# Performance work log

Measured on AMD Instinct MI355X. Metric: run time of the kernel, lower is better.

Reference implementation:

```python
import jax, jax.numpy as jnp
import numpy as np

NUM_HEADS = 16
EPS = 1e-5


def setup_inputs() -> dict:
    key = jax.random.key(0)
    ks = jax.random.split(key, 9)
    B, S, D = 2, 2048, 1024
    s = 1.0 / np.sqrt(D)
    return {
        "x": jax.random.normal(ks[0], (B, S, D), dtype=jnp.float32),
        "Wq": jax.random.uniform(ks[1], (D, D), jnp.float32, -s, s),
        "bq": jax.random.uniform(ks[2], (D,), jnp.float32, -s, s),
        "Wk": jax.random.uniform(ks[3], (D, D), jnp.float32, -s, s),
        "bk": jax.random.uniform(ks[4], (D,), jnp.float32, -s, s),
        "Wv": jax.random.uniform(ks[5], (D, D), jnp.float32, -s, s),
        "bv": jax.random.uniform(ks[6], (D,), jnp.float32, -s, s),
        "Wo": jax.random.uniform(ks[7], (D, D), jnp.float32, -s, s),
        "bo": jax.random.uniform(ks[8], (D,), jnp.float32, -s, s),
    }


def reference(x, Wq, bq, Wk, bk, Wv, bv, Wo, bo):
    B, S, D = x.shape
    H = NUM_HEADS
    hd = D // H
    # projections -> [B, H, S, hd]
    def proj(W, b):
        return (x @ W + b).reshape(B, S, H, hd).transpose(0, 2, 1, 3)
    Q = proj(Wq, bq)
    K = proj(Wk, bk)
    V = proj(Wv, bv)
    scores = jnp.einsum("bhqd,bhkd->bhqk", Q, K) / jnp.sqrt(jnp.float32(hd))
    attn = jax.nn.softmax(scores, axis=-1)  # dropout is identity in eval mode
    out = jnp.einsum("bhqk,bhkd->bhqd", attn, V)
    out = out.transpose(0, 2, 1, 3).reshape(B, S, D)
    out = jax.nn.relu(out @ Wo + bo)
    mu = jnp.mean(out, axis=-1, keepdims=True)
    var = jnp.var(out, axis=-1, keepdims=True)
    return (out - mu) * jax.lax.rsqrt(var + EPS)
```

## Files before the change

kernel.cpp:

```cpp
#include <hip/hip_runtime.h>
#include <hip/hip_bf16.h>
#include <math.h>

#define Bb 2
#define Ss 2048
#define Dd 1024
#define Hh 16
#define HD 64
#define Mm (Bb*Ss)

typedef __attribute__((ext_vector_type(8))) short bf8_t;
typedef __attribute__((ext_vector_type(4))) float f4_t;
typedef __attribute__((ext_vector_type(2))) unsigned u2_t;

#define LOG2E 1.4426950408889634f

#define AS1 __attribute__((address_space(1)))
#define AS3 __attribute__((address_space(3)))

__device__ __forceinline__ void gl2lds16(const void* g, void* l) {
    __builtin_amdgcn_global_load_lds((const AS1 unsigned int*)g,
                                     (AS3 unsigned int*)l, 16, 0, 0);
}
__device__ __forceinline__ short bfr(float f) {
    __hip_bfloat16 h = __float2bfloat16(f);
    return *reinterpret_cast<short*>(&h);
}
__device__ __forceinline__ unsigned pkbf16(float a, float b) {
    const unsigned ua = __builtin_bit_cast(unsigned, a) + 0x8000u;
    const unsigned ub = __builtin_bit_cast(unsigned, b) + 0x8000u;
    return __builtin_amdgcn_perm(ub, ua, 0x07060302u);
}
__device__ __forceinline__ float fexp2(float x) {
    return __builtin_amdgcn_exp2f(x);
}

__global__ __launch_bounds__(256)
void prep(const float* __restrict__ x,
          const float* __restrict__ w0, const float* __restrict__ w1,
          const float* __restrict__ w2, const float* __restrict__ w3,
          __hip_bfloat16* __restrict__ Wt4, __hip_bfloat16* __restrict__ Xh)
{
    const int z = blockIdx.z;
    if (z < 4) {
        const float* W = (z == 0) ? w0 : (z == 1) ? w1 : (z == 2) ? w2 : w3;
        __hip_bfloat16* Wt = Wt4 + (size_t)z * Dd * Dd;
        __shared__ float t[32][33];
        const int n0 = blockIdx.x * 32, k0 = blockIdx.y * 32;
        const int tx = threadIdx.x & 31, ty = threadIdx.x >> 5;
        #pragma unroll
        for (int rr = 0; rr < 4; ++rr)
            t[ty + rr*8][tx] = W[(size_t)(k0 + ty + rr*8) * Dd + n0 + tx];
        __syncthreads();
        #pragma unroll
        for (int rr = 0; rr < 4; ++rr)
            Wt[(size_t)(n0 + ty + rr*8) * Dd + k0 + tx] =
                __float2bfloat16(t[tx][ty + rr*8]);
    } else {
        const int bid = (z - 4) * 1024 + blockIdx.y * 32 + blockIdx.x;
        const size_t i = ((size_t)bid * 256 + threadIdx.x) * 8;
        const float4 a = *(const float4*)&x[i];
        const float4 b = *(const float4*)&x[i + 4];
        bf8_t o;
        o[0] = bfr(a.x); o[1] = bfr(a.y); o[2] = bfr(a.z); o[3] = bfr(a.w);
        o[4] = bfr(b.x); o[5] = bfr(b.y); o[6] = bfr(b.z); o[7] = bfr(b.w);
        *(bf8_t*)&Xh[i] = o;
    }
}

__global__ __launch_bounds__(256)
void gemm_qkv(const __hip_bfloat16* __restrict__ A,
              const __hip_bfloat16* __restrict__ Bt,
              const float* __restrict__ b0, const float* __restrict__ b1,
              const float* __restrict__ b2,
              __hip_bfloat16* __restrict__ Qh, __hip_bfloat16* __restrict__ Kh,
              __hip_bfloat16* __restrict__ Vt)
{
    __shared__ __align__(16) char pool[34816];
    __hip_bfloat16* As = (__hip_bfloat16*)pool;
    __hip_bfloat16* Bs = As + 2 * 128 * 32;

    const int tid  = threadIdx.x;
    const int wave = tid >> 6;
    const int lane = tid & 63;
    const int llo  = lane & 15;
    const int lhi  = lane >> 4;
    const int wm   = wave & 1;
    const int wn   = wave >> 1;
    const int row0 = blockIdx.y * 128;
    const int col0 = blockIdx.x * 128;

    size_t aoff[2], boff[2];
    int    loff[2];
    #pragma unroll
    for (int p = 0; p < 2; ++p) {
        const int g = p * 256 + wave * 64 + lane;
        const int r = g >> 2, kc = (g & 3) * 8;
        aoff[p] = (size_t)(row0 + r) * Dd + kc;
        boff[p] = (size_t)(col0 + r) * Dd + kc;
        loff[p] = (p * 256 + wave * 64) * 16;
    }
    const __hip_bfloat16* Acur = A;
    const __hip_bfloat16* Bcur = Bt;

    auto stage = [&](int buf) {
        #pragma unroll
        for (int p = 0; p < 2; ++p) {
            gl2lds16(Acur + aoff[p], (char*)As + buf*8192 + loff[p]);
            gl2lds16(Bcur + boff[p], (char*)Bs + buf*8192 + loff[p]);
        }
        Acur += 32; Bcur += 32;
    };

    f4_t acc[4][4] = {};
    stage(0);
    for (int kt = 0; kt < 32; ++kt) {
        const int buf = kt & 1;
        __syncthreads();
        if (kt + 1 < 32) stage(buf ^ 1);

        bf8_t a[4], b[4];
        #pragma unroll
        for (int i = 0; i < 4; ++i)
            a[i] = *(const bf8_t*)&As[buf*4096 + (wm*64 + i*16 + llo) * 32 + lhi*8];
        #pragma unroll
        for (int j = 0; j < 4; ++j)
            b[j] = *(const bf8_t*)&Bs[buf*4096 + (wn*64 + j*16 + llo) * 32 + lhi*8];
        #pragma unroll
        for (int i = 0; i < 4; ++i)
            #pragma unroll
            for (int j = 0; j < 4; ++j)
                acc[i][j] = __builtin_amdgcn_mfma_f32_16x16x32_bf16(
                    a[i], b[j], acc[i][j], 0, 0, 0);
    }

    const int sel   = col0 >> 10;
    const int cbase = col0 & 1023;
    if (sel < 2) {
        const float scale = (sel == 0) ? 0.125f * LOG2E : 1.0f;
        const float* bp = (sel == 0) ? b0 : b1;
        __hip_bfloat16* outQK = (sel == 0) ? Qh : Kh;
        #pragma unroll
        for (int i = 0; i < 4; ++i) {
            #pragma unroll
            for (int r = 0; r < 4; ++r) {
                const int m  = row0 + wm*64 + i*16 + lhi*4 + r;
                const int b_ = m >> 11, s_ = m & (Ss - 1);
                #pragma unroll
                for (int j = 0; j < 4; ++j) {
                    const int col = cbase + wn*64 + j*16 + llo;
                    const int h_  = col >> 6, e_ = col & 63;
                    const float v = (acc[i][j][r] + bp[col]) * scale;
                    outQK[((size_t)(b_*Hh + h_)*Ss + s_)*HD + e_] = __float2bfloat16(v);
                }
            }
        }
    } else {
        __syncthreads();
        __hip_bfloat16* Ls = (__hip_bfloat16*)pool;
        float bv[4];
        #pragma unroll
        for (int j = 0; j < 4; ++j) bv[j] = b2[cbase + wn*64 + j*16 + llo];
        #pragma unroll
        for (int i = 0; i < 4; ++i)
            #pragma unroll
            for (int r = 0; r < 4; ++r) {
                const int ml = wm*64 + i*16 + lhi*4 + r;
                #pragma unroll
                for (int j = 0; j < 4; ++j)
                    Ls[(wn*64 + j*16 + llo)*136 + ml] =
                        __float2bfloat16(acc[i][j][r] + bv[j]);
            }
        __syncthreads();
        const int b_ = row0 >> 11;
        const int sb = row0 & (Ss - 1);
        #pragma unroll
        for (int p = 0; p < 8; ++p) {
            const int cl = p*16 + (tid >> 4);
            const int m  = (tid & 15) * 8;
            const bf8_t v = *(const bf8_t*)&Ls[cl*136 + m];
            const int cc = cbase + cl;
            *(bf8_t*)&Vt[((size_t)(b_*Hh + (cc >> 6))*HD + (cc & 63))*Ss + sb + m] = v;
        }
    }
}

__global__ __launch_bounds__(128, 2)
void attn_mfma(const __hip_bfloat16* __restrict__ Qh,
               const __hip_bfloat16* __restrict__ Kh,
               const __hip_bfloat16* __restrict__ Vt,
               __hip_bfloat16* __restrict__ Ah)
{
    const int b    = blockIdx.z;
    const int h    = blockIdx.y;
    const int wave = threadIdx.x >> 6;
    const int lane = threadIdx.x & 63;
    const int llo  = lane & 15;
    const int lhi  = lane >> 4;
    const int qb   = blockIdx.x * 64 + wave * 32;

    const size_t base = ((size_t)(b*Hh + h)) * Ss * HD;

    __shared__ __hip_bfloat16 Ks[2][2 * 64 * 32];
    __shared__ __hip_bfloat16 Vs[2][2 * 64 * 32];
    __shared__ __hip_bfloat16 Pl[2][32 * 64];
    __hip_bfloat16* Pw = &Pl[wave][0];

    int koff[4], voff[4], loff[4];
    #pragma unroll
    for (int it = 0; it < 4; ++it) {
        const int g  = it*128 + wave*64 + lane;
        const int hf = g >> 8;
        const int rr = (g >> 2) & 63;
        const int c8 = (g & 3) * 8;
        koff[it] = rr*HD + hf*32 + c8;
        voff[it] = rr*Ss + hf*32 + c8;
        loff[it] = (it*128 + wave*64) * 16;
    }
    const __hip_bfloat16* Kcur = Kh + base;
    const __hip_bfloat16* Vcur = Vt + base;

    auto stage = [&](int buf) {
        #pragma unroll
        for (int it = 0; it < 4; ++it) {
            gl2lds16(Kcur + koff[it], (char*)&Ks[buf][0] + loff[it]);
            gl2lds16(Vcur + voff[it], (char*)&Vs[buf][0] + loff[it]);
        }
        Kcur += 64 * HD;
        Vcur += 64;
    };

    bf8_t qf[2][2];
    #pragma unroll
    for (int s = 0; s < 2; ++s)
        #pragma unroll
        for (int d = 0; d < 2; ++d)
            qf[s][d] = *(const bf8_t*)&Qh[base + (size_t)(qb + 16*s + llo)*HD + 32*d + lhi*8];

    f4_t o_[2][4];
    float lacc[2];
    #pragma unroll
    for (int s = 0; s < 2; ++s) {
        #pragma unroll
        for (int n = 0; n < 4; ++n) o_[s][n] = (f4_t){0.f,0.f,0.f,0.f};
        lacc[s] = 0.f;
    }

    const f4_t zf = {0.f,0.f,0.f,0.f};
    const int llo7 = llo & 7;

    stage(0);

    for (int t = 0; t < Ss/64; ++t) {
        const int buf = t & 1;
        __syncthreads();
        if (t + 1 < Ss/64) stage(buf ^ 1);

        bf8_t kf[4][2];
        #pragma unroll
        for (int kc = 0; kc < 4; ++kc)
            #pragma unroll
            for (int d = 0; d < 2; ++d)
                kf[kc][d] = *(const bf8_t*)&Ks[buf][d*2048 + (kc*16 + llo)*32 + lhi*8];

        f4_t sacc[2][4];
        #pragma unroll
        for (int s = 0; s < 2; ++s)
            #pragma unroll
            for (int kc = 0; kc < 4; ++kc) {
                sacc[s][kc] = __builtin_amdgcn_mfma_f32_16x16x32_bf16(kf[kc][0], qf[s][0], zf, 0, 0, 0);
                sacc[s][kc] = __builtin_amdgcn_mfma_f32_16x16x32_bf16(kf[kc][1], qf[s][1], sacc[s][kc], 0, 0, 0);
            }

        #pragma unroll
        for (int s = 0; s < 2; ++s) {
            #pragma unroll
            for (int kc = 0; kc < 4; ++kc) {
                const float p0 = fexp2(sacc[s][kc][0]);
                const float p1 = fexp2(sacc[s][kc][1]);
                const float p2 = fexp2(sacc[s][kc][2]);
                const float p3 = fexp2(sacc[s][kc][3]);
                lacc[s] += (p0 + p1) + (p2 + p3);
                const u2_t pk = { pkbf16(p0, p1), pkbf16(p2, p3) };
                const int phys = (2*kc + (lhi >> 1)) ^ llo7;
                *(u2_t*)&Pw[(16*s + llo)*64 + phys*8 + (lhi & 1)*4] = pk;
            }
        }
        asm volatile("s_waitcnt lgkmcnt(0)" ::: "memory");

        #pragma unroll
        for (int d = 0; d < 2; ++d) {
            bf8_t pf[2];
            #pragma unroll
            for (int s = 0; s < 2; ++s)
                pf[s] = *(const bf8_t*)&Pw[(16*s + llo)*64 + (((4*d + lhi) ^ llo7) << 3)];
            #pragma unroll
            for (int nc = 0; nc < 4; ++nc) {
                const bf8_t vf = *(const bf8_t*)&Vs[buf][d*2048 + (nc*16 + llo)*32 + lhi*8];
                #pragma unroll
                for (int s = 0; s < 2; ++s)
                    o_[s][nc] = __builtin_amdgcn_mfma_f32_16x16x32_bf16(pf[s], vf, o_[s][nc], 0, 0, 0);
            }
        }
    }

    #pragma unroll
    for (int s = 0; s < 2; ++s) {
        lacc[s] += __shfl_xor(lacc[s], 16);
        lacc[s] += __shfl_xor(lacc[s], 32);
    }

    #pragma unroll
    for (int s = 0; s < 2; ++s) {
        #pragma unroll
        for (int r = 0; r < 4; ++r) {
            const float lv  = __shfl(lacc[s], 4*lhi + r);
            const float inv = 1.0f / lv;
            const int q = qb + 16*s + 4*lhi + r;
            __hip_bfloat16* orow = &Ah[((size_t)(b*Ss) + q)*Dd + h*HD + llo];
            #pragma unroll
            for (int nc = 0; nc < 4; ++nc)
                orow[16*nc] = __float2bfloat16(o_[s][nc][r] * inv);
        }
    }
}

__global__ __launch_bounds__(256)
void gemm_out(const __hip_bfloat16* __restrict__ A,
              const __hip_bfloat16* __restrict__ Bt,
              const float* __restrict__ bias, float* __restrict__ Ro)
{
    __shared__ __hip_bfloat16 As[2][64 * 32];
    __shared__ __hip_bfloat16 Bs[2][64 * 32];

    const int tid  = threadIdx.x;
    const int wave = tid >> 6;
    const int lane = tid & 63;
    const int llo  = lane & 15;
    const int lhi  = lane >> 4;
    const int wm   = wave & 1;
    const int wn   = wave >> 1;
    const int row0 = blockIdx.y * 64;
    const int col0 = blockIdx.x * 64;

    const int gr = tid >> 2, gkc = (tid & 3) * 8;
    const size_t aoff = (size_t)(row0 + gr) * Dd + gkc;
    const size_t boff = (size_t)(col0 + gr) * Dd + gkc;
    const int loff = (wave * 64) * 16;
    const __hip_bfloat16* Acur = A;
    const __hip_bfloat16* Bcur = Bt;

    auto stage = [&](int buf) {
        gl2lds16(Acur + aoff, (char*)&As[buf][0] + loff);
        gl2lds16(Bcur + boff, (char*)&Bs[buf][0] + loff);
        Acur += 32; Bcur += 32;
    };

    f4_t acc[2][2] = {};
    stage(0);
    for (int kt = 0; kt < 32; ++kt) {
        const int buf = kt & 1;
        __syncthreads();
        if (kt + 1 < 32) stage(buf ^ 1);

        bf8_t a[2], b[2];
        #pragma unroll
        for (int i = 0; i < 2; ++i)
            a[i] = *(const bf8_t*)&As[buf][(wm*32 + i*16 + llo) * 32 + lhi*8];
        #pragma unroll
        for (int j = 0; j < 2; ++j)
            b[j] = *(const bf8_t*)&Bs[buf][(wn*32 + j*16 + llo) * 32 + lhi*8];
        #pragma unroll
        for (int i = 0; i < 2; ++i)
            #pragma unroll
            for (int j = 0; j < 2; ++j)
                acc[i][j] = __builtin_amdgcn_mfma_f32_16x16x32_bf16(
                    a[i], b[j], acc[i][j], 0, 0, 0);
    }

    #pragma unroll
    for (int i = 0; i < 2; ++i) {
        #pragma unroll
        for (int r = 0; r < 4; ++r) {
            const int m = row0 + wm*32 + i*16 + lhi*4 + r;
            #pragma unroll
            for (int j = 0; j < 2; ++j) {
                const int col = col0 + wn*32 + j*16 + llo;
                Ro[(size_t)m * Dd + col] = fmaxf(acc[i][j][r] + bias[col], 0.0f);
            }
        }
    }
}

__global__ __launch_bounds__(256)
void layernorm(const float* __restrict__ X, float* __restrict__ out)
{
    const int row = blockIdx.x;
    const float4 v = ((const float4*)(X + (size_t)row*Dd))[threadIdx.x];
    float s  = v.x + v.y + v.z + v.w;
    float ss = v.x*v.x + v.y*v.y + v.z*v.z + v.w*v.w;
    #pragma unroll
    for (int off = 32; off > 0; off >>= 1) {
        s  += __shfl_down(s,  off);
        ss += __shfl_down(ss, off);
    }
    __shared__ float rs[4], rss[4];
    const int wid = threadIdx.x >> 6, lid = threadIdx.x & 63;
    if (lid == 0) { rs[wid] = s; rss[wid] = ss; }
    __syncthreads();
    s  = rs[0] + rs[1] + rs[2] + rs[3];
    ss = rss[0] + rss[1] + rss[2] + rss[3];
    const float mean = s * (1.0f / Dd);
    const float var  = ss * (1.0f / Dd) - mean * mean;
    const float rstd = rsqrtf(var + 1e-5f);
    float4 o;
    o.x = (v.x - mean) * rstd;
    o.y = (v.y - mean) * rstd;
    o.z = (v.z - mean) * rstd;
    o.w = (v.w - mean) * rstd;
    ((float4*)(out + (size_t)row*Dd))[threadIdx.x] = o;
}

extern "C" void kernel_launch(void* const* d_in, const int* in_sizes, int n_in,
                              void* d_out, int out_size, void* d_ws, size_t ws_size,
                              hipStream_t stream)
{
    const float* x  = (const float*)d_in[0];
    const float* Wq = (const float*)d_in[1];
    const float* bq = (const float*)d_in[2];
    const float* Wk = (const float*)d_in[3];
    const float* bk = (const float*)d_in[4];
    const float* Wv = (const float*)d_in[5];
    const float* bv = (const float*)d_in[6];
    const float* Wo = (const float*)d_in[7];
    const float* bo = (const float*)d_in[8];
    float* out = (float*)d_out;

    __hip_bfloat16* Xh    = (__hip_bfloat16*)d_ws;
    __hip_bfloat16* Wqkvt = Xh    + (size_t)Mm*Dd;
    __hip_bfloat16* Wot   = Wqkvt + (size_t)3*Dd*Dd;
    __hip_bfloat16* Ah    = Wot   + (size_t)Dd*Dd;
    __hip_bfloat16* Qh    = Ah    + (size_t)Mm*Dd;
    __hip_bfloat16* Kh    = Qh    + (size_t)Mm*Dd;
    __hip_bfloat16* Vt    = Kh    + (size_t)Mm*Dd;
    float*          Rb    = (float*)Qh;

    prep<<<dim3(32, 32, 6), dim3(256), 0, stream>>>(x, Wq, Wk, Wv, Wo, Wqkvt, Xh);
    gemm_qkv<<<dim3(3*Dd/128, Mm/128), dim3(256), 0, stream>>>(
        Xh, Wqkvt, bq, bk, bv, Qh, Kh, Vt);
    attn_mfma<<<dim3(Ss/64, Hh, Bb), dim3(128), 0, stream>>>(Qh, Kh, Vt, Ah);
    gemm_out<<<dim3(Dd/64, Mm/64), dim3(256), 0, stream>>>(Ah, Wot, bo, Rb);
    layernorm<<<dim3(Mm), dim3(256), 0, stream>>>(Rb, out);
}
```

Measured before the change: 221.5 us.

## Shrink attention tiles to 16 queries per wave and stage Q/K output via LDS

The attention kernel now gives each wave 16 query rows instead of 32 and steps through keys in 32-wide tiles instead of 64. This halves LDS and register use per block, allowing more resident blocks (launch bound raised to 4) and twice as many blocks in the grid. The cost is less reuse of K/V per load and twice as many loop iterations and barriers. Separately, the QKV GEMM epilogue for Q and K now goes through a shared-memory transpose so global stores are 16-byte vectors rather than scattered 2-byte writes.

```diff
diff --git a/kernel.cpp b/kernel.cpp
--- a/kernel.cpp
+++ b/kernel.cpp
@@ -136,31 +136,40 @@
 
     const int sel   = col0 >> 10;
     const int cbase = col0 & 1023;
+    __hip_bfloat16* Ls = (__hip_bfloat16*)pool;
+    __syncthreads();
+
+    float bv[4];
+    const float* bp = (sel == 0) ? b0 : (sel == 1) ? b1 : b2;
+    #pragma unroll
+    for (int j = 0; j < 4; ++j) bv[j] = bp[cbase + wn*64 + j*16 + llo];
+    const float scale = (sel == 0) ? 0.125f * LOG2E : 1.0f;
+
     if (sel < 2) {
-        const float scale = (sel == 0) ? 0.125f * LOG2E : 1.0f;
-        const float* bp = (sel == 0) ? b0 : b1;
+        #pragma unroll
+        for (int i = 0; i < 4; ++i)
+            #pragma unroll
+            for (int r = 0; r < 4; ++r) {
+                const int ml = wm*64 + i*16 + lhi*4 + r;
+                #pragma unroll
+                for (int j = 0; j < 4; ++j)
+                    Ls[ml*136 + wn*64 + j*16 + llo] =
+                        __float2bfloat16((acc[i][j][r] + bv[j]) * scale);
+            }
+        __syncthreads();
         __hip_bfloat16* outQK = (sel == 0) ? Qh : Kh;
         #pragma unroll
-        for (int i = 0; i < 4; ++i) {
-            #pragma unroll
-            for (int r = 0; r < 4; ++r) {
-                const int m  = row0 + wm*64 + i*16 + lhi*4 + r;
-                const int b_ = m >> 11, s_ = m & (Ss - 1);
-                #pragma unroll
-                for (int j = 0; j < 4; ++j) {
-                    const int col = cbase + wn*64 + j*16 + llo;
-                    const int h_  = col >> 6, e_ = col & 63;
-                    const float v = (acc[i][j][r] + bp[col]) * scale;
-                    outQK[((size_t)(b_*Hh + h_)*Ss + s_)*HD + e_] = __float2bfloat16(v);
-                }
-            }
+        for (int p = 0; p < 8; ++p) {
+            const int id = p*256 + tid;
+            const int rl = id >> 4;
+            const int c8 = (id & 15) * 8;
+            const bf8_t v = *(const bf8_t*)&Ls[rl*136 + c8];
+            const int m  = row0 + rl;
+            const int b_ = m >> 11, s_ = m & (Ss - 1);
+            const int col = cbase + c8;
+            *(bf8_t*)&outQK[((size_t)(b_*Hh + (col >> 6))*Ss + s_)*HD + (col & 63)] = v;
         }
     } else {
-        __syncthreads();
-        __hip_bfloat16* Ls = (__hip_bfloat16*)pool;
-        float bv[4];
-        #pragma unroll
-        for (int j = 0; j < 4; ++j) bv[j] = b2[cbase + wn*64 + j*16 + llo];
         #pragma unroll
         for (int i = 0; i < 4; ++i)
             #pragma unroll
@@ -185,7 +194,7 @@
     }
 }
 
-__global__ __launch_bounds__(128, 2)
+__global__ __launch_bounds__(128, 4)
 void attn_mfma(const __hip_bfloat16* __restrict__ Qh,
                const __hip_bfloat16* __restrict__ Kh,
                const __hip_bfloat16* __restrict__ Vt,
@@ -197,24 +206,21 @@
     const int lane = threadIdx.x & 63;
     const int llo  = lane & 15;
     const int lhi  = lane >> 4;
-    const int qb   = blockIdx.x * 64 + wave * 32;
+    const int qb   = blockIdx.x * 32 + wave * 16;
 
     const size_t base = ((size_t)(b*Hh + h)) * Ss * HD;
 
-    __shared__ __hip_bfloat16 Ks[2][2 * 64 * 32];
-    __shared__ __hip_bfloat16 Vs[2][2 * 64 * 32];
-    __shared__ __hip_bfloat16 Pl[2][32 * 64];
+    __shared__ __hip_bfloat16 Ks[2][2 * 32 * 32];
+    __shared__ __hip_bfloat16 Vs[2][64 * 32];
+    __shared__ __hip_bfloat16 Pl[2][16 * 36];
     __hip_bfloat16* Pw = &Pl[wave][0];
 
-    int koff[4], voff[4], loff[4];
-    #pragma unroll
-    for (int it = 0; it < 4; ++it) {
-        const int g  = it*128 + wave*64 + lane;
-        const int hf = g >> 8;
-        const int rr = (g >> 2) & 63;
-        const int c8 = (g & 3) * 8;
-        koff[it] = rr*HD + hf*32 + c8;
-        voff[it] = rr*Ss + hf*32 + c8;
+    int koff[2], voff[2], loff[2];
+    #pragma unroll
+    for (int it = 0; it < 2; ++it) {
+        const int g = it*128 + wave*64 + lane;
+        koff[it] = ((g >> 2) & 31)*HD + (g >> 7)*32 + (g & 3)*8;
+        voff[it] = (g >> 2)*Ss + (g & 3)*8;
         loff[it] = (it*128 + wave*64) * 16;
     }
     const __hip_bfloat16* Kcur = Kh + base;
@@ -222,106 +228,79 @@
 
     auto stage = [&](int buf) {
         #pragma unroll
-        for (int it = 0; it < 4; ++it) {
+        for (int it = 0; it < 2; ++it) {
             gl2lds16(Kcur + koff[it], (char*)&Ks[buf][0] + loff[it]);
             gl2lds16(Vcur + voff[it], (char*)&Vs[buf][0] + loff[it]);
         }
-        Kcur += 64 * HD;
-        Vcur += 64;
+        Kcur += 32 * HD;
+        Vcur += 32;
     };
 
-    bf8_t qf[2][2];
-    #pragma unroll
-    for (int s = 0; s < 2; ++s)
-        #pragma unroll
-        for (int d = 0; d < 2; ++d)
-            qf[s][d] = *(const bf8_t*)&Qh[base + (size_t)(qb + 16*s + llo)*HD + 32*d + lhi*8];
-
-    f4_t o_[2][4];
-    float lacc[2];
-    #pragma unroll
-    for (int s = 0; s < 2; ++s) {
-        #pragma unroll
-        for (int n = 0; n < 4; ++n) o_[s][n] = (f4_t){0.f,0.f,0.f,0.f};
-        lacc[s] = 0.f;
-    }
+    bf8_t qf[2];
+    #pragma unroll
+    for (int d = 0; d < 2; ++d)
+        qf[d] = *(const bf8_t*)&Qh[base + (size_t)(qb + llo)*HD + 32*d + lhi*8];
+
+    f4_t o_[4];
+    float lacc = 0.f;
+    #pragma unroll
+    for (int n = 0; n < 4; ++n) o_[n] = (f4_t){0.f,0.f,0.f,0.f};
 
     const f4_t zf = {0.f,0.f,0.f,0.f};
-    const int llo7 = llo & 7;
 
     stage(0);
 
-    for (int t = 0; t < Ss/64; ++t) {
+    for (int t = 0; t < Ss/32; ++t) {
         const int buf = t & 1;
         __syncthreads();
-        if (t + 1 < Ss/64) stage(buf ^ 1);
-
-        bf8_t kf[4][2];
-        #pragma unroll
-        for (int kc = 0; kc < 4; ++kc)
+        if (t + 1 < Ss/32) stage(buf ^ 1);
+
+        bf8_t kf[2][2];
+        #pragma unroll
+        for (int kc = 0; kc < 2; ++kc)
             #pragma unroll
             for (int d = 0; d < 2; ++d)
-                kf[kc][d] = *(const bf8_t*)&Ks[buf][d*2048 + (kc*16 + llo)*32 + lhi*8];
-
-        f4_t sacc[2][4];
-        #pragma unroll
-        for (int s = 0; s < 2; ++s)
-            #pragma unroll
-            for (int kc = 0; kc < 4; ++kc) {
-                sacc[s][kc] = __builtin_amdgcn_mfma_f32_16x16x32_bf16(kf[kc][0], qf[s][0], zf, 0, 0, 0);
-                sacc[s][kc] = __builtin_amdgcn_mfma_f32_16x16x32_bf16(kf[kc][1], qf[s][1], sacc[s][kc], 0, 0, 0);
-            }
-
-        #pragma unroll
-        for (int s = 0; s < 2; ++s) {
-            #pragma unroll
-            for (int kc = 0; kc < 4; ++kc) {
-                const float p0 = fexp2(sacc[s][kc][0]);
-                const float p1 = fexp2(sacc[s][kc][1]);
-                const float p2 = fexp2(sacc[s][kc][2]);
-                const float p3 = fexp2(sacc[s][kc][3]);
-                lacc[s] += (p0 + p1) + (p2 + p3);
-                const u2_t pk = { pkbf16(p0, p1), pkbf16(p2, p3) };
-                const int phys = (2*kc + (lhi >> 1)) ^ llo7;
-                *(u2_t*)&Pw[(16*s + llo)*64 + phys*8 + (lhi & 1)*4] = pk;
-            }
+                kf[kc][d] = *(const bf8_t*)&Ks[buf][d*1024 + (kc*16 + llo)*32 + lhi*8];
+
+        f4_t sacc[2];
+        #pragma unroll
+        for (int kc = 0; kc < 2; ++kc) {
+            sacc[kc] = __builtin_amdgcn_mfma_f32_16x16x32_bf16(kf[kc][0], qf[0], zf, 0, 0, 0);
+            sacc[kc] = __builtin_amdgcn_mfma_f32_16x16x32_bf16(kf[kc][1], qf[1], sacc[kc], 0, 0, 0);
+        }
+
+        #pragma unroll
+        for (int kc = 0; kc < 2; ++kc) {
+            const float p0 = fexp2(sacc[kc][0]);
+            const float p1 = fexp2(sacc[kc][1]);
+            const float p2 = fexp2(sacc[kc][2]);
+            const float p3 = fexp2(sacc[kc][3]);
+            lacc += (p0 + p1) + (p2 + p3);
+            const u2_t pk = { pkbf16(p0, p1), pkbf16(p2, p3) };
+            *(u2_t*)&Pw[llo*36 + kc*16 + lhi*4] = pk;
         }
         asm volatile("s_waitcnt lgkmcnt(0)" ::: "memory");
 
-        #pragma unroll
-        for (int d = 0; d < 2; ++d) {
-            bf8_t pf[2];
-            #pragma unroll
-            for (int s = 0; s < 2; ++s)
-                pf[s] = *(const bf8_t*)&Pw[(16*s + llo)*64 + (((4*d + lhi) ^ llo7) << 3)];
-            #pragma unroll
-            for (int nc = 0; nc < 4; ++nc) {
-                const bf8_t vf = *(const bf8_t*)&Vs[buf][d*2048 + (nc*16 + llo)*32 + lhi*8];
-                #pragma unroll
-                for (int s = 0; s < 2; ++s)
-                    o_[s][nc] = __builtin_amdgcn_mfma_f32_16x16x32_bf16(pf[s], vf, o_[s][nc], 0, 0, 0);
-            }
-        }
-    }
-
-    #pragma unroll
-    for (int s = 0; s < 2; ++s) {
-        lacc[s] += __shfl_xor(lacc[s], 16);
-        lacc[s] += __shfl_xor(lacc[s], 32);
-    }
-
-    #pragma unroll
-    for (int s = 0; s < 2; ++s) {
-        #pragma unroll
-        for (int r = 0; r < 4; ++r) {
-            const float lv  = __shfl(lacc[s], 4*lhi + r);
-            const float inv = 1.0f / lv;
-            const int q = qb + 16*s + 4*lhi + r;
-            __hip_bfloat16* orow = &Ah[((size_t)(b*Ss) + q)*Dd + h*HD + llo];
-            #pragma unroll
-            for (int nc = 0; nc < 4; ++nc)
-                orow[16*nc] = __float2bfloat16(o_[s][nc][r] * inv);
-        }
+        const bf8_t pf = *(const bf8_t*)&Pw[llo*36 + lhi*8];
+        #pragma unroll
+        for (int nc = 0; nc < 4; ++nc) {
+            const bf8_t vf = *(const bf8_t*)&Vs[buf][(nc*16 + llo)*32 + lhi*8];
+            o_[nc] = __builtin_amdgcn_mfma_f32_16x16x32_bf16(pf, vf, o_[nc], 0, 0, 0);
+        }
+    }
+
+    lacc += __shfl_xor(lacc, 16);
+    lacc += __shfl_xor(lacc, 32);
+
+    #pragma unroll
+    for (int r = 0; r < 4; ++r) {
+        const float lv  = __shfl(lacc, 4*lhi + r);
+        const float inv = 1.0f / lv;
+        const int q = qb + 4*lhi + r;
+        __hip_bfloat16* orow = &Ah[((size_t)(b*Ss) + q)*Dd + h*HD + llo];
+        #pragma unroll
+        for (int nc = 0; nc < 4; ++nc)
+            orow[16*nc] = __float2bfloat16(o_[nc][r] * inv);
     }
 }
 
@@ -448,7 +427,7 @@
     prep<<<dim3(32, 32, 6), dim3(256), 0, stream>>>(x, Wq, Wk, Wv, Wo, Wqkvt, Xh);
     gemm_qkv<<<dim3(3*Dd/128, Mm/128), dim3(256), 0, stream>>>(
         Xh, Wqkvt, bq, bk, bv, Qh, Kh, Vt);
-    attn_mfma<<<dim3(Ss/64, Hh, Bb), dim3(128), 0, stream>>>(Qh, Kh, Vt, Ah);
+    attn_mfma<<<dim3(Ss/32, Hh, Bb), dim3(128), 0, stream>>>(Qh, Kh, Vt, Ah);
     gemm_out<<<dim3(Dd/64, Mm/64), dim3(256), 0, stream>>>(Ah, Wot, bo, Rb);
     layernorm<<<dim3(Mm), dim3(256), 0, stream>>>(Rb, out);
 }
```

Result: slower. 239.8 us (+8.3%).

## Stage Q/K stores via LDS and split-K retile output GEMM with fused epilogue

Applied to the files above, without the earlier changes.

The Q/K epilogue of the QKV GEMM now goes through an LDS transpose buffer, so each thread writes 16-byte coalesced vectors into the head-major layout instead of scattered scalar stores. The output projection moves from 64x64 to 128x128 tiles with a two-way split-K over blockIdx.z. Each split writes raw fp32 partials, and layernorm sums them and applies bias and ReLU. This improves data reuse and store coalescing, at the cost of extra partial-sum traffic and more workspace.

```diff
diff --git a/kernel.cpp b/kernel.cpp
--- a/kernel.cpp
+++ b/kernel.cpp
@@ -136,31 +136,40 @@
 
     const int sel   = col0 >> 10;
     const int cbase = col0 & 1023;
+    __hip_bfloat16* Ls = (__hip_bfloat16*)pool;
+    __syncthreads();
+
+    float bv[4];
+    const float* bp = (sel == 0) ? b0 : (sel == 1) ? b1 : b2;
+    #pragma unroll
+    for (int j = 0; j < 4; ++j) bv[j] = bp[cbase + wn*64 + j*16 + llo];
+    const float scale = (sel == 0) ? 0.125f * LOG2E : 1.0f;
+
     if (sel < 2) {
-        const float scale = (sel == 0) ? 0.125f * LOG2E : 1.0f;
-        const float* bp = (sel == 0) ? b0 : b1;
+        #pragma unroll
+        for (int i = 0; i < 4; ++i)
+            #pragma unroll
+            for (int r = 0; r < 4; ++r) {
+                const int ml = wm*64 + i*16 + lhi*4 + r;
+                #pragma unroll
+                for (int j = 0; j < 4; ++j)
+                    Ls[ml*136 + wn*64 + j*16 + llo] =
+                        __float2bfloat16((acc[i][j][r] + bv[j]) * scale);
+            }
+        __syncthreads();
         __hip_bfloat16* outQK = (sel == 0) ? Qh : Kh;
         #pragma unroll
-        for (int i = 0; i < 4; ++i) {
-            #pragma unroll
-            for (int r = 0; r < 4; ++r) {
-                const int m  = row0 + wm*64 + i*16 + lhi*4 + r;
-                const int b_ = m >> 11, s_ = m & (Ss - 1);
-                #pragma unroll
-                for (int j = 0; j < 4; ++j) {
-                    const int col = cbase + wn*64 + j*16 + llo;
-                    const int h_  = col >> 6, e_ = col & 63;
-                    const float v = (acc[i][j][r] + bp[col]) * scale;
-                    outQK[((size_t)(b_*Hh + h_)*Ss + s_)*HD + e_] = __float2bfloat16(v);
-                }
-            }
+        for (int p = 0; p < 8; ++p) {
+            const int id = p*256 + tid;
+            const int rl = id >> 4;
+            const int c8 = (id & 15) * 8;
+            const bf8_t v = *(const bf8_t*)&Ls[rl*136 + c8];
+            const int m  = row0 + rl;
+            const int b_ = m >> 11, s_ = m & (Ss - 1);
+            const int col = cbase + c8;
+            *(bf8_t*)&outQK[((size_t)(b_*Hh + (col >> 6))*Ss + s_)*HD + (col & 63)] = v;
         }
     } else {
-        __syncthreads();
-        __hip_bfloat16* Ls = (__hip_bfloat16*)pool;
-        float bv[4];
-        #pragma unroll
-        for (int j = 0; j < 4; ++j) bv[j] = b2[cbase + wn*64 + j*16 + llo];
         #pragma unroll
         for (int i = 0; i < 4; ++i)
             #pragma unroll
@@ -328,10 +337,10 @@
 __global__ __launch_bounds__(256)
 void gemm_out(const __hip_bfloat16* __restrict__ A,
               const __hip_bfloat16* __restrict__ Bt,
-              const float* __restrict__ bias, float* __restrict__ Ro)
-{
-    __shared__ __hip_bfloat16 As[2][64 * 32];
-    __shared__ __hip_bfloat16 Bs[2][64 * 32];
+              float* __restrict__ Ro)
+{
+    __shared__ __hip_bfloat16 As[2][128 * 32];
+    __shared__ __hip_bfloat16 Bs[2][128 * 32];
 
     const int tid  = threadIdx.x;
     const int wave = tid >> 6;
@@ -340,63 +349,84 @@
     const int lhi  = lane >> 4;
     const int wm   = wave & 1;
     const int wn   = wave >> 1;
-    const int row0 = blockIdx.y * 64;
-    const int col0 = blockIdx.x * 64;
-
-    const int gr = tid >> 2, gkc = (tid & 3) * 8;
-    const size_t aoff = (size_t)(row0 + gr) * Dd + gkc;
-    const size_t boff = (size_t)(col0 + gr) * Dd + gkc;
-    const int loff = (wave * 64) * 16;
-    const __hip_bfloat16* Acur = A;
-    const __hip_bfloat16* Bcur = Bt;
+    const int row0 = blockIdx.y * 128;
+    const int col0 = blockIdx.x * 128;
+    const int z    = blockIdx.z;
+
+    size_t aoff[2], boff[2];
+    int    loff[2];
+    #pragma unroll
+    for (int p = 0; p < 2; ++p) {
+        const int g = p * 256 + wave * 64 + lane;
+        const int r = g >> 2, kc = (g & 3) * 8;
+        aoff[p] = (size_t)(row0 + r) * Dd + kc;
+        boff[p] = (size_t)(col0 + r) * Dd + kc;
+        loff[p] = (p * 256 + wave * 64) * 16;
+    }
+    const __hip_bfloat16* Acur = A  + (size_t)z * (Dd/2);
+    const __hip_bfloat16* Bcur = Bt + (size_t)z * (Dd/2);
 
     auto stage = [&](int buf) {
-        gl2lds16(Acur + aoff, (char*)&As[buf][0] + loff);
-        gl2lds16(Bcur + boff, (char*)&Bs[buf][0] + loff);
+        #pragma unroll
+        for (int p = 0; p < 2; ++p) {
+            gl2lds16(Acur + aoff[p], (char*)&As[buf][0] + loff[p]);
+            gl2lds16(Bcur + boff[p], (char*)&Bs[buf][0] + loff[p]);
+        }
         Acur += 32; Bcur += 32;
     };
 
-    f4_t acc[2][2] = {};
+    f4_t acc[4][4] = {};
     stage(0);
-    for (int kt = 0; kt < 32; ++kt) {
+    for (int kt = 0; kt < 16; ++kt) {
         const int buf = kt & 1;
         __syncthreads();
-        if (kt + 1 < 32) stage(buf ^ 1);
-
-        bf8_t a[2], b[2];
-        #pragma unroll
-        for (int i = 0; i < 2; ++i)
-            a[i] = *(const bf8_t*)&As[buf][(wm*32 + i*16 + llo) * 32 + lhi*8];
-        #pragma unroll
-        for (int j = 0; j < 2; ++j)
-            b[j] = *(const bf8_t*)&Bs[buf][(wn*32 + j*16 + llo) * 32 + lhi*8];
-        #pragma unroll
-        for (int i = 0; i < 2; ++i)
-            #pragma unroll
-            for (int j = 0; j < 2; ++j)
+        if (kt + 1 < 16) stage(buf ^ 1);
+
+        bf8_t a[4], b[4];
+        #pragma unroll
+        for (int i = 0; i < 4; ++i)
+            a[i] = *(const bf8_t*)&As[buf][(wm*64 + i*16 + llo) * 32 + lhi*8];
+        #pragma unroll
+        for (int j = 0; j < 4; ++j)
+            b[j] = *(const bf8_t*)&Bs[buf][(wn*64 + j*16 + llo) * 32 + lhi*8];
+        #pragma unroll
+        for (int i = 0; i < 4; ++i)
+            #pragma unroll
+            for (int j = 0; j < 4; ++j)
                 acc[i][j] = __builtin_amdgcn_mfma_f32_16x16x32_bf16(
                     a[i], b[j], acc[i][j], 0, 0, 0);
     }
 
-    #pragma unroll
-    for (int i = 0; i < 2; ++i) {
+    float* Roz = Ro + (size_t)z * Mm * Dd;
+    #pragma unroll
+    for (int i = 0; i < 4; ++i) {
         #pragma unroll
         for (int r = 0; r < 4; ++r) {
-            const int m = row0 + wm*32 + i*16 + lhi*4 + r;
-            #pragma unroll
-            for (int j = 0; j < 2; ++j) {
-                const int col = col0 + wn*32 + j*16 + llo;
-                Ro[(size_t)m * Dd + col] = fmaxf(acc[i][j][r] + bias[col], 0.0f);
+            const int m = row0 + wm*64 + i*16 + lhi*4 + r;
+            #pragma unroll
+            for (int j = 0; j < 4; ++j) {
+                const int col = col0 + wn*64 + j*16 + llo;
+                Roz[(size_t)m * Dd + col] = acc[i][j][r];
             }
         }
     }
 }
 
 __global__ __launch_bounds__(256)
-void layernorm(const float* __restrict__ X, float* __restrict__ out)
+void layernorm(const float* __restrict__ P0, const float* __restrict__ P1,
+               const float* __restrict__ bias, float* __restrict__ out)
 {
     const int row = blockIdx.x;
-    const float4 v = ((const float4*)(X + (size_t)row*Dd))[threadIdx.x];
+    const int c = threadIdx.x;
+    const float4 a  = ((const float4*)(P0 + (size_t)row*Dd))[c];
+    const float4 b  = ((const float4*)(P1 + (size_t)row*Dd))[c];
+    const float4 bb = ((const float4*)bias)[c];
+    float4 v;
+    v.x = fmaxf(a.x + b.x + bb.x, 0.0f);
+    v.y = fmaxf(a.y + b.y + bb.y, 0.0f);
+    v.z = fmaxf(a.z + b.z + bb.z, 0.0f);
+    v.w = fmaxf(a.w + b.w + bb.w, 0.0f);
+
     float s  = v.x + v.y + v.z + v.w;
     float ss = v.x*v.x + v.y*v.y + v.z*v.z + v.w*v.w;
     #pragma unroll
@@ -405,7 +435,7 @@
         ss += __shfl_down(ss, off);
     }
     __shared__ float rs[4], rss[4];
-    const int wid = threadIdx.x >> 6, lid = threadIdx.x & 63;
+    const int wid = c >> 6, lid = c & 63;
     if (lid == 0) { rs[wid] = s; rss[wid] = ss; }
     __syncthreads();
     s  = rs[0] + rs[1] + rs[2] + rs[3];
@@ -418,7 +448,7 @@
     o.y = (v.y - mean) * rstd;
     o.z = (v.z - mean) * rstd;
     o.w = (v.w - mean) * rstd;
-    ((float4*)(out + (size_t)row*Dd))[threadIdx.x] = o;
+    ((float4*)(out + (size_t)row*Dd))[c] = o;
 }
 
 extern "C" void kernel_launch(void* const* d_in, const int* in_sizes, int n_in,
@@ -449,6 +479,6 @@
     gemm_qkv<<<dim3(3*Dd/128, Mm/128), dim3(256), 0, stream>>>(
         Xh, Wqkvt, bq, bk, bv, Qh, Kh, Vt);
     attn_mfma<<<dim3(Ss/64, Hh, Bb), dim3(128), 0, stream>>>(Qh, Kh, Vt, Ah);
-    gemm_out<<<dim3(Dd/64, Mm/64), dim3(256), 0, stream>>>(Ah, Wot, bo, Rb);
-    layernorm<<<dim3(Mm), dim3(256), 0, stream>>>(Rb, out);
-}
+    gemm_out<<<dim3(Dd/128, Mm/128, 2), dim3(256), 0, stream>>>(Ah, Wot, Rb);
+    layernorm<<<dim3(Mm), dim3(256), 0, stream>>>(Rb, Rb + (size_t)Mm*Dd, bo, out);
+}
```

Result: faster. 215.1 us (-2.9%).
